# Performance work log

Hardware: AMD Instinct MI355X
Metric: run time of the kernel (lower is better)

The kernel has to match this reference:

```python
import jax, jax.numpy as jnp
import numpy as np

N, F = 2048, 128
HEADS, OUT_DIM = 8, 8
ALPHA = 0.2  # tf.nn.leaky_relu default


def setup_inputs() -> dict:
    key = jax.random.key(0)
    k1, k2, k3, k4 = jax.random.split(key, 4)
    X = jax.random.normal(k1, (N, F), dtype=jnp.float32)
    A = jax.random.randint(k2, (N, N), 0, 2, dtype=jnp.int32)
    W = jax.random.normal(k3, (F, OUT_DIM * HEADS), dtype=jnp.float32) * (1.0 / np.sqrt(F))
    attn_kernel = jax.random.normal(k4, (2 * OUT_DIM, 1), dtype=jnp.float32) * 0.1
    return {"X": X, "A": A, "W": W, "attn_kernel": attn_kernel}


def reference(X, A, W, attn_kernel):
    # h: [N, heads, out_dim]
    h = (X @ W).reshape(N, HEADS, OUT_DIM)
    # tensordot(concat(h_i, h_j), a) == h_i @ a1 + h_j @ a2 (linear before leaky_relu),
    # so avoid materializing the [N,N,heads,2*out_dim] tile-concat tensor.
    a1 = attn_kernel[:OUT_DIM, 0]
    a2 = attn_kernel[OUT_DIM:, 0]
    s1 = jnp.einsum('nhd,d->nh', h, a1)  # [N, heads]
    s2 = jnp.einsum('nhd,d->nh', h, a2)  # [N, heads]
    e = jax.nn.leaky_relu(s1[:, None, :] + s2[None, :, :], ALPHA)  # [N, N, heads]
    mask = (A > 0).astype(e.dtype)[:, :, None]
    e = e * mask - 1e9 * (1.0 - mask)
    attention = jax.nn.softmax(e, axis=1)  # softmax over neighbor axis (axis=1), as in source
    # Faithful to source: einsum 'nij,njh->nih' contracts the HEAD axis
    # (attention [N,N,heads] with h [N,heads,out_dim]) -> [N, N, out_dim]
    h_prime = jnp.einsum('nij,njh->nih', attention, h)
    h_prime = h_prime.reshape(-1, OUT_DIM * HEADS)  # [N*N/heads, out_dim*heads]
    return jax.nn.leaky_relu(h_prime, ALPHA)
```

## Files before the change

kernel.cpp:

```cpp
#include <hip/hip_runtime.h>
#include <hip/hip_bf16.h>

#define NN      2048
#define FDIM    128
#define HEADS   8
#define ODIM    8
#define HID     64
#define ALPHA   0.2f

__device__ __forceinline__ float lrelu(float x) {
    return x > 0.f ? x : ALPHA * x;
}

__global__ __launch_bounds__(64) void gat_prep(
        const float* __restrict__ X,
        const float* __restrict__ W,
        const float* __restrict__ ak,
        float* __restrict__ H,
        float* __restrict__ S1,
        float* __restrict__ S2) {
    const int n = blockIdx.x;
    const int t = threadIdx.x;

    __shared__ float Xs[FDIM];
    __shared__ float hs[HID];

    Xs[t]      = X[(size_t)n * FDIM + t];
    Xs[t + 64] = X[(size_t)n * FDIM + 64 + t];
    __syncthreads();

    float acc = 0.f;
    #pragma unroll 8
    for (int k = 0; k < FDIM; ++k)
        acc = fmaf(Xs[k], W[k * HID + t], acc);

    H[(size_t)n * HID + t] = acc;
    hs[t] = acc;
    __syncthreads();

    if (t < 16) {
        const int head = t & 7;
        const float* a = ak + ((t < 8) ? 0 : ODIM);
        float s = 0.f;
        #pragma unroll
        for (int d = 0; d < ODIM; ++d)
            s = fmaf(hs[head * ODIM + d], a[d], s);
        if (t < 8) S1[n * HEADS + head] = s;
        else       S2[n * HEADS + head] = s;
    }
}

__global__ __launch_bounds__(512) void gat_rowsum(
        const int*   __restrict__ A,
        const float* __restrict__ S1,
        const float* __restrict__ S2,
        float* __restrict__ LF) {
    const int i    = blockIdx.x;
    const int t    = threadIdx.x;
    const int wave = t >> 6;
    const int lane = t & 63;

    __shared__ int   As[NN];
    __shared__ float redL[8 * HEADS];

    const int4* Arow4 = (const int4*)(A + (size_t)i * NN);
    ((int4*)As)[t] = Arow4[t];

    float s1r[HEADS];
    #pragma unroll
    for (int h = 0; h < HEADS; ++h) s1r[h] = S1[i * HEADS + h];

    __syncthreads();

    float ls[HEADS];
    #pragma unroll
    for (int h = 0; h < HEADS; ++h) ls[h] = 0.f;

    #pragma unroll
    for (int jj = 0; jj < 4; ++jj) {
        const int j = t + jj * 512;
        const float4 s2a = *(const float4*)(S2 + j * HEADS);
        const float4 s2b = *(const float4*)(S2 + j * HEADS + 4);
        const bool msk = As[j] > 0;
        const float s2v[8] = {s2a.x, s2a.y, s2a.z, s2a.w,
                              s2b.x, s2b.y, s2b.z, s2b.w};
        #pragma unroll
        for (int h = 0; h < HEADS; ++h) {
            const float x = s1r[h] + s2v[h];
            ls[h] += msk ? __expf(lrelu(x)) : 0.f;
        }
    }

    #pragma unroll
    for (int h = 0; h < HEADS; ++h) {
        float v = ls[h];
        #pragma unroll
        for (int off = 32; off; off >>= 1)
            v += __shfl_xor(v, off);
        if (lane == 0) redL[wave * HEADS + h] = v;
    }
    __syncthreads();

    if (t < HEADS) {
        float v = 0.f;
        #pragma unroll
        for (int w = 0; w < 8; ++w)
            v += redL[w * HEADS + t];
        LF[i * HEADS + t] = v;
    }
}

__global__ __launch_bounds__(256, 4) void gat_write(
        const int*   __restrict__ A,
        const float* __restrict__ H,
        const float* __restrict__ S1,
        const float* __restrict__ S2,
        const float* __restrict__ LF,
        float* __restrict__ out) {
    const int i = blockIdx.x;
    const int t = threadIdx.x;

    __shared__ int   As[NN];
    __shared__ float hhS[HID];

    const int4* Arow4 = (const int4*)(A + (size_t)i * NN);
    ((int4*)As)[t]       = Arow4[t];
    ((int4*)As)[t + 256] = Arow4[t + 256];

    if (t < HID)
        hhS[t] = H[(size_t)i * HID + t] / LF[i * HEADS + (t >> 3)];

    float s1r[HEADS];
    #pragma unroll
    for (int h = 0; h < HEADS; ++h) s1r[h] = S1[i * HEADS + h];

    __syncthreads();

    float hh[HID];
    #pragma unroll
    for (int k = 0; k < HID; k += 4) {
        const float4 v = *(const float4*)(hhS + k);
        hh[k] = v.x; hh[k + 1] = v.y; hh[k + 2] = v.z; hh[k + 3] = v.w;
    }

    #pragma unroll
    for (int jj = 0; jj < 8; ++jj) {
        const int j = t + jj * 256;
        const float4 s2a = *(const float4*)(S2 + j * HEADS);
        const float4 s2b = *(const float4*)(S2 + j * HEADS + 4);
        const bool msk = As[j] > 0;
        const float s2v[8] = {s2a.x, s2a.y, s2a.z, s2a.w,
                              s2b.x, s2b.y, s2b.z, s2b.w};

        float p[HEADS];
        #pragma unroll
        for (int h = 0; h < HEADS; ++h) {
            const float x = s1r[h] + s2v[h];
            p[h] = msk ? __expf(lrelu(x)) : 0.f;
        }

        float o[ODIM];
        #pragma unroll
        for (int d = 0; d < ODIM; ++d) o[d] = 0.f;
        #pragma unroll
        for (int h = 0; h < HEADS; ++h) {
            #pragma unroll
            for (int d = 0; d < ODIM; ++d)
                o[d] = fmaf(p[h], hh[h * ODIM + d], o[d]);
        }

        const size_t base = ((size_t)i * NN + j) * ODIM;
        float4 o0, o1;
        o0.x = lrelu(o[0]); o0.y = lrelu(o[1]);
        o0.z = lrelu(o[2]); o0.w = lrelu(o[3]);
        o1.x = lrelu(o[4]); o1.y = lrelu(o[5]);
        o1.z = lrelu(o[6]); o1.w = lrelu(o[7]);
        *(float4*)(out + base)     = o0;
        *(float4*)(out + base + 4) = o1;
    }
}

extern "C" void kernel_launch(void* const* d_in, const int* in_sizes, int n_in,
                              void* d_out, int out_size, void* d_ws, size_t ws_size,
                              hipStream_t stream) {
    const float* X  = (const float*)d_in[0];
    const int*   A  = (const int*)  d_in[1];
    const float* W  = (const float*)d_in[2];
    const float* ak = (const float*)d_in[3];
    float* out = (float*)d_out;

    float* H  = (float*)d_ws;
    float* S1 = H  + (size_t)NN * HID;
    float* S2 = S1 + (size_t)NN * HEADS;
    float* LF = S2 + (size_t)NN * HEADS;

    gat_prep  <<<NN,  64, 0, stream>>>(X, W, ak, H, S1, S2);
    gat_rowsum<<<NN, 512, 0, stream>>>(A, S1, S2, LF);
    gat_write <<<NN, 256, 0, stream>>>(A, H, S1, S2, LF, out);
}
```

Baseline: 179.0 us.

## Pack adjacency mask into bitmask and use nontemporal output stores

The rowsum kernel now reads A directly, builds a 64-bit ballot bitmask per wave and writes it to workspace. The write kernel reads that bitmask instead of re-reading the full 16 MB int adjacency matrix, and drops the shared-memory staging and block sync. The output is written with nontemporal stores to avoid polluting cache with the 128 MB result. The normalization is also folded into registers via reciprocals. This adds a small workspace buffer and depends on the workspace being large enough.

```diff
diff --git a/kernel.cpp b/kernel.cpp
--- a/kernel.cpp
+++ b/kernel.cpp
@@ -7,6 +7,9 @@
 #define ODIM    8
 #define HID     64
 #define ALPHA   0.2f
+#define NWORDS  (NN / 64)
+
+typedef float vfloat4 __attribute__((ext_vector_type(4)));
 
 __device__ __forceinline__ float lrelu(float x) {
     return x > 0.f ? x : ALPHA * x;
@@ -54,23 +57,18 @@
         const int*   __restrict__ A,
         const float* __restrict__ S1,
         const float* __restrict__ S2,
-        float* __restrict__ LF) {
+        float* __restrict__ LF,
+        unsigned long long* __restrict__ Mb) {
     const int i    = blockIdx.x;
     const int t    = threadIdx.x;
     const int wave = t >> 6;
     const int lane = t & 63;
 
-    __shared__ int   As[NN];
     __shared__ float redL[8 * HEADS];
 
-    const int4* Arow4 = (const int4*)(A + (size_t)i * NN);
-    ((int4*)As)[t] = Arow4[t];
-
     float s1r[HEADS];
     #pragma unroll
     for (int h = 0; h < HEADS; ++h) s1r[h] = S1[i * HEADS + h];
-
-    __syncthreads();
 
     float ls[HEADS];
     #pragma unroll
@@ -79,9 +77,13 @@
     #pragma unroll
     for (int jj = 0; jj < 4; ++jj) {
         const int j = t + jj * 512;
+        const bool msk = A[(size_t)i * NN + j] > 0;
+
+        const unsigned long long b = __ballot(msk);
+        if (lane == 0) Mb[i * NWORDS + wave + jj * 8] = b;
+
         const float4 s2a = *(const float4*)(S2 + j * HEADS);
         const float4 s2b = *(const float4*)(S2 + j * HEADS + 4);
-        const bool msk = As[j] > 0;
         const float s2v[8] = {s2a.x, s2a.y, s2a.z, s2a.w,
                               s2b.x, s2b.y, s2b.z, s2b.w};
         #pragma unroll
@@ -111,44 +113,46 @@
 }
 
 __global__ __launch_bounds__(256, 4) void gat_write(
-        const int*   __restrict__ A,
+        const unsigned long long* __restrict__ Mb,
         const float* __restrict__ H,
         const float* __restrict__ S1,
         const float* __restrict__ S2,
         const float* __restrict__ LF,
         float* __restrict__ out) {
-    const int i = blockIdx.x;
-    const int t = threadIdx.x;
-
-    __shared__ int   As[NN];
-    __shared__ float hhS[HID];
-
-    const int4* Arow4 = (const int4*)(A + (size_t)i * NN);
-    ((int4*)As)[t]       = Arow4[t];
-    ((int4*)As)[t + 256] = Arow4[t + 256];
-
-    if (t < HID)
-        hhS[t] = H[(size_t)i * HID + t] / LF[i * HEADS + (t >> 3)];
-
+    const int i    = blockIdx.x;
+    const int t    = threadIdx.x;
+    const int wave = t >> 6;
+    const int lane = t & 63;
+
+    float lfr[HEADS];
+    {
+        const float4 l0 = *(const float4*)(LF + i * HEADS);
+        const float4 l1 = *(const float4*)(LF + i * HEADS + 4);
+        lfr[0] = 1.f / l0.x; lfr[1] = 1.f / l0.y;
+        lfr[2] = 1.f / l0.z; lfr[3] = 1.f / l0.w;
+        lfr[4] = 1.f / l1.x; lfr[5] = 1.f / l1.y;
+        lfr[6] = 1.f / l1.z; lfr[7] = 1.f / l1.w;
+    }
+    float hh[HID];
+    #pragma unroll
+    for (int k = 0; k < HID; k += 4) {
+        const float4 v = *(const float4*)(H + (size_t)i * HID + k);
+        const float r = lfr[k >> 3];
+        hh[k]     = v.x * r; hh[k + 1] = v.y * r;
+        hh[k + 2] = v.z * r; hh[k + 3] = v.w * r;
+    }
     float s1r[HEADS];
     #pragma unroll
     for (int h = 0; h < HEADS; ++h) s1r[h] = S1[i * HEADS + h];
-
-    __syncthreads();
-
-    float hh[HID];
-    #pragma unroll
-    for (int k = 0; k < HID; k += 4) {
-        const float4 v = *(const float4*)(hhS + k);
-        hh[k] = v.x; hh[k + 1] = v.y; hh[k + 2] = v.z; hh[k + 3] = v.w;
-    }
 
     #pragma unroll
     for (int jj = 0; jj < 8; ++jj) {
         const int j = t + jj * 256;
+        const unsigned long long m = Mb[i * NWORDS + wave + jj * 4];
+        const bool msk = (m >> lane) & 1ull;
+
         const float4 s2a = *(const float4*)(S2 + j * HEADS);
         const float4 s2b = *(const float4*)(S2 + j * HEADS + 4);
-        const bool msk = As[j] > 0;
         const float s2v[8] = {s2a.x, s2a.y, s2a.z, s2a.w,
                               s2b.x, s2b.y, s2b.z, s2b.w};
 
@@ -170,13 +174,13 @@
         }
 
         const size_t base = ((size_t)i * NN + j) * ODIM;
-        float4 o0, o1;
+        vfloat4 o0, o1;
         o0.x = lrelu(o[0]); o0.y = lrelu(o[1]);
         o0.z = lrelu(o[2]); o0.w = lrelu(o[3]);
         o1.x = lrelu(o[4]); o1.y = lrelu(o[5]);
         o1.z = lrelu(o[6]); o1.w = lrelu(o[7]);
-        *(float4*)(out + base)     = o0;
-        *(float4*)(out + base + 4) = o1;
+        __builtin_nontemporal_store(o0, (vfloat4*)(out + base));
+        __builtin_nontemporal_store(o1, (vfloat4*)(out + base + 4));
     }
 }
 
@@ -193,8 +197,9 @@
     float* S1 = H  + (size_t)NN * HID;
     float* S2 = S1 + (size_t)NN * HEADS;
     float* LF = S2 + (size_t)NN * HEADS;
+    unsigned long long* Mb = (unsigned long long*)(LF + (size_t)NN * HEADS);
 
     gat_prep  <<<NN,  64, 0, stream>>>(X, W, ak, H, S1, S2);
-    gat_rowsum<<<NN, 512, 0, stream>>>(A, S1, S2, LF);
-    gat_write <<<NN, 256, 0, stream>>>(A, H, S1, S2, LF, out);
-}
+    gat_rowsum<<<NN, 512, 0, stream>>>(A, S1, S2, LF, Mb);
+    gat_write <<<NN, 256, 0, stream>>>(Mb, H, S1, S2, LF, out);
+}
```

Result: slower. 224.9 us (+25.7%).
